# Performance work log

Measured on AMD Instinct MI355X. Metric: run time of the kernel, lower is better.

Reference implementation:

```python
import jax, jax.numpy as jnp
import numpy as np

S = 4096   # decoder sequence length
T = 4096   # encoder sequence length
D = 2048   # x_size == qk_size (required for q @ k^T to typecheck)


def setup_inputs() -> dict:
    key = jax.random.key(0)
    k1, k2, k3, k4 = jax.random.split(key, 4)
    x_vectors = jax.random.normal(k1, (S, D), dtype=jnp.float32)
    enc_output = jax.random.normal(k2, (2, T, S), dtype=jnp.float32) * 0.02
    Wq = jax.random.normal(k3, (D, D), dtype=jnp.float32) * 0.02
    bq = jax.random.normal(k4, (D,), dtype=jnp.float32) * 0.02
    return {"x_vectors": x_vectors, "enc_output": enc_output, "Wq": Wq, "bq": bq}


def reference(x_vectors, enc_output, Wq, bq):
    # q = Linear(x): [S, D]
    q = x_vectors @ Wq.T + bq
    # k, v produced by matmul of encoder-output matrices with x: [T, D]
    k = enc_output[0] @ x_vectors
    v = enc_output[1] @ x_vectors
    # attention scores [S, T], scaled by sqrt(qk_size)
    e = (q @ k.T) / jnp.sqrt(jnp.float32(D))
    # softmax over dim=1 (last axis of the rank-2 score matrix)
    a = jax.nn.softmax(e, axis=1)
    # z = a @ v^T: [S, D]
    z = a @ v
    return z
```

## Files before the change

kernel.cpp:

```cpp
#include <hip/hip_runtime.h>


typedef __attribute__((ext_vector_type(8))) __bf16 bf16x8;
typedef __attribute__((ext_vector_type(4))) float f32x4;
typedef __attribute__((ext_vector_type(4))) unsigned short ushort4v;
typedef __attribute__((ext_vector_type(8))) unsigned short ushort8v;

#define S_DIM 4096
#define T_DIM 4096
#define D_DIM 2048

__device__ __forceinline__ unsigned short f2bf(float f) {
    unsigned int u = __float_as_uint(f);
    u += 0x7fffu + ((u >> 16) & 1u);
    return (unsigned short)(u >> 16);
}

__device__ __forceinline__ void block_sync() {
    __builtin_amdgcn_sched_barrier(0);
    __builtin_amdgcn_s_barrier();
    __builtin_amdgcn_sched_barrier(0);
}

#define GL(gptr, sptr)                                                        \
    __builtin_amdgcn_global_load_lds(                                         \
        (__attribute__((address_space(1))) void*)(void*)(gptr),               \
        (__attribute__((address_space(3))) void*)(sptr), 16, 0, 0)

__global__ __launch_bounds__(256)
void k_convert(const float* __restrict__ in, unsigned short* __restrict__ out, long n) {
    long i = ((long)blockIdx.x * blockDim.x + threadIdx.x) * 8;
    const long stride = (long)gridDim.x * blockDim.x * 8;
    for (; i < n; i += stride) {
        float4 a = *(const float4*)(in + i);
        float4 b = *(const float4*)(in + i + 4);
        ushort8v o;
        o[0] = f2bf(a.x); o[1] = f2bf(a.y); o[2] = f2bf(a.z); o[3] = f2bf(a.w);
        o[4] = f2bf(b.x); o[5] = f2bf(b.y); o[6] = f2bf(b.z); o[7] = f2bf(b.w);
        *(ushort8v*)(out + i) = o;
    }
}

__global__ __launch_bounds__(256)
void k_transpose(const float* __restrict__ in, unsigned short* __restrict__ out,
                 int R, int C) {
    __shared__ float tile[32][33];
    const int bx = blockIdx.x * 32;
    const int by = blockIdx.y * 32;
    const int tx = threadIdx.x;
    const int ty = threadIdx.y;
    #pragma unroll
    for (int i = 0; i < 32; i += 8)
        tile[ty + i][tx] = in[(long)(by + ty + i) * C + bx + tx];
    __syncthreads();
    #pragma unroll
    for (int i = 0; i < 32; i += 8)
        out[(long)(bx + ty + i) * R + by + tx] = f2bf(tile[tx][ty + i]);
}

template<int BM, int OUT_BF16, int HAS_BIAS>
__global__ __launch_bounds__(512, 2)
void k_gemm(const unsigned short* __restrict__ A,
            const unsigned short* __restrict__ B,
            const float* __restrict__ bias,
            void* __restrict__ C,
            int M, int N, int K, float alpha) {
    constexpr int MFR    = BM / 32;
    constexpr int AGRAN  = BM * 4;
    constexpr int ALOADS = AGRAN / 512;
    constexpr int LDSA   = AGRAN * 16;
    constexpr int BUF    = LDSA + 16384;
    extern __shared__ __align__(16) char smem[];

    const int tid = threadIdx.x;
    const int l = tid & 63;
    const int w = tid >> 6;
    const int wr = w >> 2;
    const int wc = w & 3;

    const int gx = gridDim.x, gy = gridDim.y;
    const int flat = blockIdx.y * gx + blockIdx.x;
    const int per = (gx * gy) >> 3;
    const int wid = (flat & 7) * per + (flat >> 3);
    const int sc = wid / (gy * 4);
    const int rm = wid - sc * gy * 4;
    const int by = rm >> 2;
    const int bx = sc * 4 + (rm & 3);

    const long brow = (long)by * BM;
    const long bcol = (long)bx * 256;
    const int NT = K >> 5;

    const unsigned short* gA[ALOADS];
    int ldA[ALOADS];
    #pragma unroll
    for (int j = 0; j < ALOADS; ++j) {
        const int q = (w * ALOADS + j) * 64 + l;
        const int R = q >> 3, s = q & 7, cp = s ^ (R & 7);
        gA[j] = A + (brow + 2 * R + (cp & 1)) * (long)K + (cp >> 1) * 8;
        ldA[j] = q * 16;
    }
    const unsigned short* gB[2];
    int ldB[2];
    #pragma unroll
    for (int j = 0; j < 2; ++j) {
        const int q = (w * 2 + j) * 64 + l;
        const int R = q >> 3, s = q & 7, cp = s ^ (R & 7);
        gB[j] = B + (bcol + 2 * R + (cp & 1)) * (long)K + (cp >> 1) * 8;
        ldB[j] = LDSA + q * 16;
    }

    const int sAB = (((((l >> 4) << 1) | (l & 1)) ^ ((l >> 1) & 7)) << 4);
    const int arB = (wr * (BM / 4) + ((l & 15) >> 1)) * 128 + sAB;
    const int brB = LDSA + (wc * 32 + ((l & 15) >> 1)) * 128 + sAB;

    f32x4 acc[MFR][4] = {};

    auto stage = [&](char* dst) {
        #pragma unroll
        for (int j = 0; j < ALOADS; ++j) { GL(gA[j], dst + ldA[j]); gA[j] += 32; }
        #pragma unroll
        for (int j = 0; j < 2; ++j)      { GL(gB[j], dst + ldB[j]); gB[j] += 32; }
    };

    {
        char* d = smem;
        #pragma unroll
        for (int tt = 0; tt < 3; ++tt) { stage(d); d += BUF; }
        if constexpr (BM == 256) asm volatile("s_waitcnt vmcnt(8)" ::: "memory");
        else                     asm volatile("s_waitcnt vmcnt(6)" ::: "memory");
        block_sync();
    }

    auto tile = [&](char* cur, char* stg, int t) {
        if (t + 3 < NT) stage(stg);
        bf16x8 bfr[4], afr[MFR];
        #pragma unroll
        for (int n = 0; n < 4; ++n)
            bfr[n] = *(const bf16x8*)(cur + brB + n * 1024);
        #pragma unroll
        for (int m = 0; m < MFR; ++m)
            afr[m] = *(const bf16x8*)(cur + arB + m * 1024);
        __builtin_amdgcn_s_setprio(1);
        #pragma unroll
        for (int m = 0; m < MFR; ++m)
            #pragma unroll
            for (int n = 0; n < 4; ++n)
                acc[m][n] = __builtin_amdgcn_mfma_f32_16x16x32_bf16(
                    afr[m], bfr[n], acc[m][n], 0, 0, 0);
        __builtin_amdgcn_s_setprio(0);
        asm volatile("s_waitcnt lgkmcnt(0)" ::: "memory");
        if (t + 3 < NT) {
            if constexpr (BM == 256) asm volatile("s_waitcnt vmcnt(8)" ::: "memory");
            else                     asm volatile("s_waitcnt vmcnt(6)" ::: "memory");
        } else if (t + 2 < NT) {
            if constexpr (BM == 256) asm volatile("s_waitcnt vmcnt(4)" ::: "memory");
            else                     asm volatile("s_waitcnt vmcnt(3)" ::: "memory");
        } else if (t + 1 < NT) {
            asm volatile("s_waitcnt vmcnt(0)" ::: "memory");
        }
        if (t + 1 < NT) block_sync();
    };

    char* b0 = smem;
    char* b1 = smem + BUF;
    char* b2 = smem + 2 * BUF;
    char* b3 = smem + 3 * BUF;
    for (int t = 0; t < NT; t += 4) {
        tile(b0, b3, t);
        tile(b1, b0, t + 1);
        tile(b2, b1, t + 2);
        tile(b3, b2, t + 3);
    }

    const long crow0 = brow + wr * (BM / 2) + (l >> 4) * 4;
    const long ccol0 = bcol + wc * 64 + (l & 15);
    #pragma unroll
    for (int n = 0; n < 4; ++n) {
        const long col = ccol0 + n * 16;
        const float bb = HAS_BIAS ? bias[col] : 0.0f;
        #pragma unroll
        for (int m = 0; m < MFR; ++m) {
            #pragma unroll
            for (int r = 0; r < 4; ++r) {
                const long row = crow0 + m * 16 + r;
                const float v = acc[m][n][r] * alpha + bb;
                if (OUT_BF16)
                    ((unsigned short*)C)[row * N + col] = f2bf(v);
                else
                    ((float*)C)[row * N + col] = v;
            }
        }
    }
}

__global__ __launch_bounds__(256)
void k_softmax(const float* __restrict__ E, unsigned short* __restrict__ A, int T) {
    const long row = blockIdx.x;
    const float* er = E + row * (long)T;
    const int t = threadIdx.x;
    const int l = t & 63;
    const int w = t >> 6;

    float4 v[4];
    float m = -3.4e38f;
    #pragma unroll
    for (int j = 0; j < 4; ++j) {
        v[j] = *(const float4*)(er + j * 1024 + t * 4);
        m = fmaxf(m, fmaxf(fmaxf(v[j].x, v[j].y), fmaxf(v[j].z, v[j].w)));
    }
    #pragma unroll
    for (int o = 32; o > 0; o >>= 1) m = fmaxf(m, __shfl_xor(m, o));

    __shared__ float redm[4];
    __shared__ float reds[4];
    if (l == 0) redm[w] = m;
    __syncthreads();
    m = fmaxf(fmaxf(redm[0], redm[1]), fmaxf(redm[2], redm[3]));

    float s = 0.f;
    #pragma unroll
    for (int j = 0; j < 4; ++j) {
        v[j].x = __expf(v[j].x - m); s += v[j].x;
        v[j].y = __expf(v[j].y - m); s += v[j].y;
        v[j].z = __expf(v[j].z - m); s += v[j].z;
        v[j].w = __expf(v[j].w - m); s += v[j].w;
    }
    #pragma unroll
    for (int o = 32; o > 0; o >>= 1) s += __shfl_xor(s, o);
    if (l == 0) reds[w] = s;
    __syncthreads();
    s = reds[0] + reds[1] + reds[2] + reds[3];
    const float inv = 1.0f / s;

    unsigned short* ar = A + row * (long)T;
    #pragma unroll
    for (int j = 0; j < 4; ++j) {
        ushort4v o4;
        o4[0] = f2bf(v[j].x * inv);
        o4[1] = f2bf(v[j].y * inv);
        o4[2] = f2bf(v[j].z * inv);
        o4[3] = f2bf(v[j].w * inv);
        *(ushort4v*)(ar + j * 1024 + t * 4) = o4;
    }
}

extern "C" void kernel_launch(void* const* d_in, const int* in_sizes, int n_in,
                              void* d_out, int out_size, void* d_ws, size_t ws_size,
                              hipStream_t stream) {
    const float* x   = (const float*)d_in[0];
    const float* enc = (const float*)d_in[1];
    const float* Wq  = (const float*)d_in[2];
    const float* bq  = (const float*)d_in[3];
    float* out = (float*)d_out;
    char* ws = (char*)d_ws;

    unsigned short* xT    = (unsigned short*)(ws);
    unsigned short* xbf   = (unsigned short*)(ws + (16L << 20));
    unsigned short* wqbf  = (unsigned short*)(ws + (32L << 20));
    unsigned short* qbf   = (unsigned short*)(ws + (40L << 20));
    unsigned short* kbf   = (unsigned short*)(ws + (56L << 20));
    unsigned short* vT    = (unsigned short*)(ws + (72L << 20));
    unsigned short* encbf = (unsigned short*)(ws + (88L << 20));
    float*          e     = (float*)(ws + (88L << 20));
    unsigned short* abf   = (unsigned short*)(ws + (152L << 20));

    k_convert<<<4096, 256, 0, stream>>>(x,   xbf,   (long)S_DIM * D_DIM);
    k_convert<<<4096, 256, 0, stream>>>(Wq,  wqbf,  (long)D_DIM * D_DIM);
    k_convert<<<4096, 256, 0, stream>>>(enc, encbf, 2L * T_DIM * S_DIM);
    k_transpose<<<dim3(D_DIM / 32, S_DIM / 32), dim3(32, 8), 0, stream>>>(x, xT, S_DIM, D_DIM);

    #define LAUNCH_G(BMV, OB, HB, Ap, Bp, biasp, Cp, M_, N_, K_, al)                       \
        do {                                                                               \
            constexpr int smemB = (BMV * 4 + 1024) * 16 * 4;                               \
            hipFuncSetAttribute((const void*)k_gemm<BMV, OB, HB>,                          \
                                hipFuncAttributeMaxDynamicSharedMemorySize, smemB);        \
            k_gemm<BMV, OB, HB><<<dim3((N_) / 256, (M_) / BMV), 512, smemB, stream>>>(     \
                Ap, Bp, biasp, Cp, M_, N_, K_, al);                                        \
        } while (0)

    LAUNCH_G(128, 1, 1, xbf, wqbf, bq, qbf, S_DIM, D_DIM, D_DIM, 1.0f);
    LAUNCH_G(128, 1, 0, encbf, xT, nullptr, kbf, T_DIM, D_DIM, S_DIM, 1.0f);
    LAUNCH_G(128, 1, 0, xT, encbf + (long)T_DIM * S_DIM, nullptr, vT, D_DIM, T_DIM, S_DIM, 1.0f);
    LAUNCH_G(256, 0, 0, qbf, kbf, nullptr, e, S_DIM, T_DIM, D_DIM, 0.022097086912079608f);
    k_softmax<<<S_DIM, 256, 0, stream>>>(e, abf, T_DIM);
    LAUNCH_G(128, 0, 0, abf, vT, nullptr, out, S_DIM, D_DIM, T_DIM, 1.0f);
}
```

Baseline: 434.0 us.

## Software-pipeline LDS fragment reads and merge K/V projection GEMMs

```diff
diff --git a/kernel.cpp b/kernel.cpp
--- a/kernel.cpp
+++ b/kernel.cpp
@@ -26,6 +26,10 @@
     __builtin_amdgcn_global_load_lds(                                         \
         (__attribute__((address_space(1))) void*)(void*)(gptr),               \
         (__attribute__((address_space(3))) void*)(sptr), 16, 0, 0)
+
+__device__ __forceinline__ f32x4 MFMA(bf16x8 a, bf16x8 b, f32x4 c) {
+    return __builtin_amdgcn_mfma_f32_16x16x32_bf16(a, b, c, 0, 0, 0);
+}
 
 __global__ __launch_bounds__(256)
 void k_convert(const float* __restrict__ in, unsigned short* __restrict__ out, long n) {
@@ -58,18 +62,92 @@
         out[(long)(bx + ty + i) * R + by + tx] = f2bf(tile[tx][ty + i]);
 }
 
-template<int BM, int OUT_BF16, int HAS_BIAS>
+__global__ __launch_bounds__(256)
+void k_transpose_bf(const unsigned short* __restrict__ in,
+                    unsigned short* __restrict__ out, int R, int C) {
+    __shared__ unsigned short tile[32][33];
+    const int bx = blockIdx.x * 32;
+    const int by = blockIdx.y * 32;
+    const int tx = threadIdx.x;
+    const int ty = threadIdx.y;
+    #pragma unroll
+    for (int i = 0; i < 32; i += 8)
+        tile[ty + i][tx] = in[(long)(by + ty + i) * C + bx + tx];
+    __syncthreads();
+    #pragma unroll
+    for (int i = 0; i < 32; i += 8)
+        out[(long)(bx + ty + i) * R + by + tx] = tile[tx][ty + i];
+}
+
+template<int MFR, bool DOSTG, bool DOREAD, int WVM, bool DOBAR, int LPTA>
+__device__ __forceinline__ void seg_t(
+    const unsigned short* (&gA)[2], const int (&ldA)[2],
+    const unsigned short* (&gB)[2], const int (&ldB)[2],
+    char* cur, char* nxt, char* stg, int arB, int brB,
+    bf16x8 (&au)[4], bf16x8 (&bu)[4], bf16x8 (&af)[4], bf16x8 (&bf_)[4],
+    f32x4 (&acc)[MFR][4])
+{
+    bf16x8 a47[4];
+    if constexpr (MFR == 8) {
+        #pragma unroll
+        for (int j = 0; j < 4; ++j)
+            a47[j] = *(const bf16x8*)(cur + arB + (4 + j) * 1024);
+    }
+    if constexpr (DOSTG) {
+        #pragma unroll
+        for (int j = 0; j < LPTA; ++j) { GL(gA[j], stg + ldA[j]); gA[j] += 32; }
+        #pragma unroll
+        for (int j = 0; j < 2; ++j)    { GL(gB[j], stg + ldB[j]); gB[j] += 32; }
+    }
+    if constexpr (DOREAD) {
+        #pragma unroll
+        for (int n = 0; n < 4; ++n)
+            bf_[n] = *(const bf16x8*)(nxt + brB + n * 1024);
+        #pragma unroll
+        for (int m = 0; m < 4; ++m)
+            af[m] = *(const bf16x8*)(nxt + arB + m * 1024);
+    }
+    if constexpr (MFR == 8 && DOREAD)  asm volatile("s_waitcnt lgkmcnt(12)" ::: "memory");
+    else if constexpr (MFR == 8)       asm volatile("s_waitcnt lgkmcnt(4)" ::: "memory");
+    else if constexpr (DOREAD)         asm volatile("s_waitcnt lgkmcnt(8)" ::: "memory");
+    else                               asm volatile("s_waitcnt lgkmcnt(0)" ::: "memory");
+    __builtin_amdgcn_sched_barrier(0);
+    __builtin_amdgcn_s_setprio(1);
+    #pragma unroll
+    for (int m = 0; m < 4; ++m)
+        #pragma unroll
+        for (int n = 0; n < 4; ++n)
+            acc[m][n] = MFMA(au[m], bu[n], acc[m][n]);
+    if constexpr (MFR == 8) {
+        if constexpr (DOREAD) asm volatile("s_waitcnt lgkmcnt(8)" ::: "memory");
+        else                  asm volatile("s_waitcnt lgkmcnt(0)" ::: "memory");
+        __builtin_amdgcn_sched_barrier(0);
+        #pragma unroll
+        for (int j = 0; j < 4; ++j)
+            #pragma unroll
+            for (int n = 0; n < 4; ++n)
+                acc[4 + j][n] = MFMA(a47[j], bu[n], acc[4 + j][n]);
+    }
+    __builtin_amdgcn_s_setprio(0);
+    if constexpr (WVM == 4)      asm volatile("s_waitcnt vmcnt(4)" ::: "memory");
+    else if constexpr (WVM == 3) asm volatile("s_waitcnt vmcnt(3)" ::: "memory");
+    else if constexpr (WVM == 0) asm volatile("s_waitcnt vmcnt(0)" ::: "memory");
+    if constexpr (DOBAR) block_sync();
+}
+
+template<int MFR, int OUT_BF16, int HAS_BIAS>
 __global__ __launch_bounds__(512, 2)
 void k_gemm(const unsigned short* __restrict__ A,
             const unsigned short* __restrict__ B,
             const float* __restrict__ bias,
             void* __restrict__ C,
             int M, int N, int K, float alpha) {
-    constexpr int MFR    = BM / 32;
-    constexpr int AGRAN  = BM * 4;
-    constexpr int ALOADS = AGRAN / 512;
-    constexpr int LDSA   = AGRAN * 16;
-    constexpr int BUF    = LDSA + 16384;
+    constexpr int BM    = MFR * 32;
+    constexpr int AGRAN = BM * 4;
+    constexpr int LPTA  = AGRAN / 512;
+    constexpr int LDSA  = AGRAN * 16;
+    constexpr int SLOT  = LDSA + 16384;
+    constexpr int LPT   = LPTA + 2;
     extern __shared__ __align__(16) char smem[];
 
     const int tid = threadIdx.x;
@@ -91,11 +169,11 @@
     const long bcol = (long)bx * 256;
     const int NT = K >> 5;
 
-    const unsigned short* gA[ALOADS];
-    int ldA[ALOADS];
-    #pragma unroll
-    for (int j = 0; j < ALOADS; ++j) {
-        const int q = (w * ALOADS + j) * 64 + l;
+    const unsigned short* gA[2];
+    int ldA[2];
+    #pragma unroll
+    for (int j = 0; j < LPTA; ++j) {
+        const int q = (w * LPTA + j) * 64 + l;
         const int R = q >> 3, s = q & 7, cp = s ^ (R & 7);
         gA[j] = A + (brow + 2 * R + (cp & 1)) * (long)K + (cp >> 1) * 8;
         ldA[j] = q * 16;
@@ -110,70 +188,54 @@
         ldB[j] = LDSA + q * 16;
     }
 
-    const int sAB = (((((l >> 4) << 1) | (l & 1)) ^ ((l >> 1) & 7)) << 4);
-    const int arB = (wr * (BM / 4) + ((l & 15) >> 1)) * 128 + sAB;
+    const int sAB = ((((l >> 4) << 1) | (l & 1)) ^ ((l & 15) >> 1)) << 4;
+    const int arB = (wr * (MFR * 8) + ((l & 15) >> 1)) * 128 + sAB;
     const int brB = LDSA + (wc * 32 + ((l & 15) >> 1)) * 128 + sAB;
 
+    char* P0 = smem;
+    char* P1 = smem + SLOT;
+    char* P2 = smem + 2 * SLOT;
+    char* P3 = smem + 3 * SLOT;
+
     f32x4 acc[MFR][4] = {};
-
-    auto stage = [&](char* dst) {
-        #pragma unroll
-        for (int j = 0; j < ALOADS; ++j) { GL(gA[j], dst + ldA[j]); gA[j] += 32; }
-        #pragma unroll
-        for (int j = 0; j < 2; ++j)      { GL(gB[j], dst + ldB[j]); gB[j] += 32; }
-    };
+    bf16x8 aE[4], bE[4], aO[4], bO[4];
 
     {
-        char* d = smem;
-        #pragma unroll
-        for (int tt = 0; tt < 3; ++tt) { stage(d); d += BUF; }
-        if constexpr (BM == 256) asm volatile("s_waitcnt vmcnt(8)" ::: "memory");
-        else                     asm volatile("s_waitcnt vmcnt(6)" ::: "memory");
+        auto stage = [&](char* dst) {
+            #pragma unroll
+            for (int j = 0; j < LPTA; ++j) { GL(gA[j], dst + ldA[j]); gA[j] += 32; }
+            #pragma unroll
+            for (int j = 0; j < 2; ++j)    { GL(gB[j], dst + ldB[j]); gB[j] += 32; }
+        };
+        stage(P0); stage(P1); stage(P2);
+        if constexpr (MFR == 8) asm volatile("s_waitcnt vmcnt(4)" ::: "memory");
+        else                    asm volatile("s_waitcnt vmcnt(3)" ::: "memory");
         block_sync();
-    }
-
-    auto tile = [&](char* cur, char* stg, int t) {
-        if (t + 3 < NT) stage(stg);
-        bf16x8 bfr[4], afr[MFR];
-        #pragma unroll
-        for (int n = 0; n < 4; ++n)
-            bfr[n] = *(const bf16x8*)(cur + brB + n * 1024);
-        #pragma unroll
-        for (int m = 0; m < MFR; ++m)
-            afr[m] = *(const bf16x8*)(cur + arB + m * 1024);
-        __builtin_amdgcn_s_setprio(1);
-        #pragma unroll
-        for (int m = 0; m < MFR; ++m)
-            #pragma unroll
-            for (int n = 0; n < 4; ++n)
-                acc[m][n] = __builtin_amdgcn_mfma_f32_16x16x32_bf16(
-                    afr[m], bfr[n], acc[m][n], 0, 0, 0);
-        __builtin_amdgcn_s_setprio(0);
-        asm volatile("s_waitcnt lgkmcnt(0)" ::: "memory");
-        if (t + 3 < NT) {
-            if constexpr (BM == 256) asm volatile("s_waitcnt vmcnt(8)" ::: "memory");
-            else                     asm volatile("s_waitcnt vmcnt(6)" ::: "memory");
-        } else if (t + 2 < NT) {
-            if constexpr (BM == 256) asm volatile("s_waitcnt vmcnt(4)" ::: "memory");
-            else                     asm volatile("s_waitcnt vmcnt(3)" ::: "memory");
-        } else if (t + 1 < NT) {
-            asm volatile("s_waitcnt vmcnt(0)" ::: "memory");
-        }
-        if (t + 1 < NT) block_sync();
-    };
-
-    char* b0 = smem;
-    char* b1 = smem + BUF;
-    char* b2 = smem + 2 * BUF;
-    char* b3 = smem + 3 * BUF;
-    for (int t = 0; t < NT; t += 4) {
-        tile(b0, b3, t);
-        tile(b1, b0, t + 1);
-        tile(b2, b1, t + 2);
-        tile(b3, b2, t + 3);
-    }
-
-    const long crow0 = brow + wr * (BM / 2) + (l >> 4) * 4;
+        #pragma unroll
+        for (int n = 0; n < 4; ++n) bE[n] = *(const bf16x8*)(P0 + brB + n * 1024);
+        #pragma unroll
+        for (int m = 0; m < 4; ++m) aE[m] = *(const bf16x8*)(P0 + arB + m * 1024);
+    }
+
+    constexpr int WVM = (MFR == 8) ? 4 : 3;
+    for (int t = 0; t + 6 <= NT; t += 2) {
+        seg_t<MFR, true, true, WVM, true, LPTA>(gA, ldA, gB, ldB, P0, P1, P3,
+                                                arB, brB, aE, bE, aO, bO, acc);
+        seg_t<MFR, true, true, WVM, true, LPTA>(gA, ldA, gB, ldB, P1, P2, P0,
+                                                arB, brB, aO, bO, aE, bE, acc);
+        char* tp = P0; P0 = P2; P2 = tp;
+        tp = P1; P1 = P3; P3 = tp;
+    }
+    seg_t<MFR, true,  true, WVM, true, LPTA>(gA, ldA, gB, ldB, P0, P1, P3,
+                                             arB, brB, aE, bE, aO, bO, acc);
+    seg_t<MFR, false, true, 0,   true, LPTA>(gA, ldA, gB, ldB, P1, P2, nullptr,
+                                             arB, brB, aO, bO, aE, bE, acc);
+    seg_t<MFR, false, true, -1,  true, LPTA>(gA, ldA, gB, ldB, P2, P3, nullptr,
+                                             arB, brB, aE, bE, aO, bO, acc);
+    seg_t<MFR, false, false, -1, false, LPTA>(gA, ldA, gB, ldB, P3, nullptr, nullptr,
+                                              arB, brB, aO, bO, aE, bE, acc);
+
+    const long crow0 = brow + wr * (MFR * 16) + (l >> 4) * 4;
     const long ccol0 = bcol + wc * 64 + (l & 15);
     #pragma unroll
     for (int n = 0; n < 4; ++n) {
@@ -255,34 +317,35 @@
     float* out = (float*)d_out;
     char* ws = (char*)d_ws;
 
+    unsigned short* abf   = (unsigned short*)(ws);
     unsigned short* xT    = (unsigned short*)(ws);
     unsigned short* xbf   = (unsigned short*)(ws + (16L << 20));
     unsigned short* wqbf  = (unsigned short*)(ws + (32L << 20));
     unsigned short* qbf   = (unsigned short*)(ws + (40L << 20));
-    unsigned short* kbf   = (unsigned short*)(ws + (56L << 20));
-    unsigned short* vT    = (unsigned short*)(ws + (72L << 20));
-    unsigned short* encbf = (unsigned short*)(ws + (88L << 20));
-    float*          e     = (float*)(ws + (88L << 20));
-    unsigned short* abf   = (unsigned short*)(ws + (152L << 20));
+    unsigned short* kv    = (unsigned short*)(ws + (56L << 20));
+    unsigned short* vT    = (unsigned short*)(ws + (88L << 20));
+    unsigned short* encbf = (unsigned short*)(ws + (104L << 20));
+    float*          e     = (float*)(ws + (104L << 20));
 
     k_convert<<<4096, 256, 0, stream>>>(x,   xbf,   (long)S_DIM * D_DIM);
     k_convert<<<4096, 256, 0, stream>>>(Wq,  wqbf,  (long)D_DIM * D_DIM);
     k_convert<<<4096, 256, 0, stream>>>(enc, encbf, 2L * T_DIM * S_DIM);
     k_transpose<<<dim3(D_DIM / 32, S_DIM / 32), dim3(32, 8), 0, stream>>>(x, xT, S_DIM, D_DIM);
 
-    #define LAUNCH_G(BMV, OB, HB, Ap, Bp, biasp, Cp, M_, N_, K_, al)                       \
+    #define LAUNCH_G(MFRV, OB, HB, Ap, Bp, biasp, Cp, M_, N_, K_, al)                      \
         do {                                                                               \
-            constexpr int smemB = (BMV * 4 + 1024) * 16 * 4;                               \
-            hipFuncSetAttribute((const void*)k_gemm<BMV, OB, HB>,                          \
+            constexpr int smemB = ((MFRV * 32 * 4) * 16 + 16384) * 4;                      \
+            hipFuncSetAttribute((const void*)k_gemm<MFRV, OB, HB>,                         \
                                 hipFuncAttributeMaxDynamicSharedMemorySize, smemB);        \
-            k_gemm<BMV, OB, HB><<<dim3((N_) / 256, (M_) / BMV), 512, smemB, stream>>>(     \
-                Ap, Bp, biasp, Cp, M_, N_, K_, al);                                        \
+            k_gemm<MFRV, OB, HB><<<dim3((N_) / 256, (M_) / (MFRV * 32)), 512, smemB,       \
+                                   stream>>>(Ap, Bp, biasp, Cp, M_, N_, K_, al);           \
         } while (0)
 
-    LAUNCH_G(128, 1, 1, xbf, wqbf, bq, qbf, S_DIM, D_DIM, D_DIM, 1.0f);
-    LAUNCH_G(128, 1, 0, encbf, xT, nullptr, kbf, T_DIM, D_DIM, S_DIM, 1.0f);
-    LAUNCH_G(128, 1, 0, xT, encbf + (long)T_DIM * S_DIM, nullptr, vT, D_DIM, T_DIM, S_DIM, 1.0f);
-    LAUNCH_G(256, 0, 0, qbf, kbf, nullptr, e, S_DIM, T_DIM, D_DIM, 0.022097086912079608f);
+    LAUNCH_G(4, 1, 1, xbf, wqbf, bq, qbf, S_DIM, D_DIM, D_DIM, 1.0f);
+    LAUNCH_G(8, 1, 0, encbf, xT, nullptr, kv, 2 * T_DIM, D_DIM, S_DIM, 1.0f);
+    k_transpose_bf<<<dim3(D_DIM / 32, T_DIM / 32), dim3(32, 8), 0, stream>>>(
+        kv + (long)T_DIM * D_DIM, vT, T_DIM, D_DIM);
+    LAUNCH_G(8, 0, 0, qbf, kv, nullptr, e, S_DIM, T_DIM, D_DIM, 0.022097086912079608f);
     k_softmax<<<S_DIM, 256, 0, stream>>>(e, abf, T_DIM);
-    LAUNCH_G(128, 0, 0, abf, vT, nullptr, out, S_DIM, D_DIM, T_DIM, 1.0f);
-}
+    LAUNCH_G(4, 0, 0, abf, vT, nullptr, out, S_DIM, D_DIM, T_DIM, 1.0f);
+}
```

Result: faster. 391.4 us (-9.8%).
